# Kernel tuning notes

Hardware: AMD Instinct MI355X
Metric: run time of the kernel (lower is better)

## Reference

```python
import jax, jax.numpy as jnp
import numpy as np


def setup_inputs() -> dict:
    key = jax.random.key(0)
    kq, kk, kv = jax.random.split(key, 3)
    B, L, H, E = 4, 2048, 16, 64
    return {
        "queries": jax.random.normal(kq, (B, L, H, E), dtype=jnp.float32),
        "keys": jax.random.normal(kk, (B, L, H, E), dtype=jnp.float32),
        "values": jax.random.normal(kv, (B, L, H, E), dtype=jnp.float32),
    }


def reference(queries, keys, values):
    B, L, H, E = queries.shape
    S = keys.shape[1]
    scale = 1.0 / jnp.sqrt(jnp.asarray(E, queries.dtype))
    # scores: [B, H, L, S]
    scores = jnp.einsum("blhe,bshe->bhls", queries, keys)
    # causal mask: disallow s > l (upper triangle, diagonal=1)
    causal = jnp.triu(jnp.ones((L, S), dtype=bool), k=1)
    scores = jnp.where(causal[None, None], -jnp.inf, scores)
    A = jax.nn.softmax(scale * scores, axis=-1)
    V = jnp.einsum("bhls,bshd->blhd", A, values)
    return V
```

## Files before the change

### kernel.cpp

```cpp
#include <hip/hip_runtime.h>
#include <hip/hip_bf16.h>

typedef __attribute__((ext_vector_type(8))) short short8;
typedef __attribute__((ext_vector_type(4))) float f32x4;
typedef __attribute__((ext_vector_type(4))) float f4;
typedef __attribute__((ext_vector_type(2))) unsigned uint2v;
typedef __attribute__((ext_vector_type(4))) unsigned uint4v;

#define MFMA(a, b, c) __builtin_amdgcn_mfma_f32_16x16x32_bf16(a, b, c, 0, 0, 0)

constexpr int B_ = 4, L = 2048, H = 16, E = 64;
constexpr int QBLK = 128, KVBLK = 64, NW = 8;
constexpr int LDP = 72;
constexpr float LOG2E = 1.4426950408889634f;
constexpr float C2 = 14.426950408889634f;
constexpr size_t NELEM = (size_t)B_ * L * H * E;
constexpr size_t WS_NEEDED = NELEM * 2 * 2;
constexpr int TILE_SHORTS = KVBLK * E;

__device__ __forceinline__ unsigned short f2bf(float f) {
  union { float f; unsigned u; } x;
  x.f = f;
  unsigned r = x.u + 0x7fffu + ((x.u >> 16) & 1u);
  return (unsigned short)(r >> 16);
}

__device__ __forceinline__ float exp2_fast(float x) {
  float r;
  asm("v_exp_f32 %0, %1" : "=v"(r) : "v"(x));
  return r;
}
__device__ __forceinline__ unsigned cvt_pk_bf16(float lo, float hi) {
  unsigned r;
  asm("v_cvt_pk_bf16_f32 %0, %1, %2" : "=v"(r) : "v"(lo), "v"(hi));
  return r;
}

__device__ __forceinline__ void gload_lds16(const void* g, void* l) {
  __builtin_amdgcn_global_load_lds(
      (const __attribute__((address_space(1))) unsigned*)g,
      (__attribute__((address_space(3))) unsigned*)l, 16, 0, 0);
}

__device__ __forceinline__ void stage_tile8(const unsigned short* gtile,
                                            unsigned short* ltile,
                                            unsigned qb, unsigned qs) {
  gload_lds16((const char*)gtile + qs, (char*)ltile + qb);
}

__device__ __forceinline__ void barrier_raw() {
  __builtin_amdgcn_sched_barrier(0);
  __builtin_amdgcn_s_barrier();
  __builtin_amdgcn_sched_barrier(0);
}

__global__ __launch_bounds__(256)
void prep_all(const float* __restrict__ K, const float* __restrict__ V,
              unsigned short* __restrict__ Kb, unsigned short* __restrict__ Vt) {
  __shared__ unsigned short Ts[E][KVBLK + 8];
  const int tid = threadIdx.x;
  if (blockIdx.y == 0) {
    const size_t t = (size_t)blockIdx.x * 256 + tid;
    const size_t row = t >> 3;
    const int e0 = ((int)t & 7) * 8;
    const int h = (int)(row % H);
    const size_t bl = row / H;
    const int l = (int)(bl % L);
    const int b = (int)(bl / L);
    f4 a = *(const f4*)(K + t * 8);
    f4 c = *(const f4*)(K + t * 8 + 4);
    short8 o;
    o[0] = (short)f2bf(a[0]); o[1] = (short)f2bf(a[1]);
    o[2] = (short)f2bf(a[2]); o[3] = (short)f2bf(a[3]);
    o[4] = (short)f2bf(c[0]); o[5] = (short)f2bf(c[1]);
    o[6] = (short)f2bf(c[2]); o[7] = (short)f2bf(c[3]);
    *(short8*)(Kb + (((size_t)b * H + h) * L + l) * E + e0) = o;
    return;
  }
  const int blk = blockIdx.x;
  if (blk >= B_ * H * (L / KVBLK)) return;
  const int st = blk % (L / KVBLK);
  const int bh = blk / (L / KVBLK);
  const int h = bh % H, b = bh / H;
  const int r = tid >> 3, e0 = (tid & 7) * 8;
  const float* vp = V + (((size_t)b * L + st * KVBLK) * H + h) * E;
#pragma unroll
  for (int rr = 0; rr < 2; ++rr) {
    const int row = rr * 32 + r;
    f4 a = *(const f4*)(vp + (size_t)row * (H * E) + e0);
    f4 c = *(const f4*)(vp + (size_t)row * (H * E) + e0 + 4);
#pragma unroll
    for (int j = 0; j < 4; ++j) Ts[e0 + j][row] = f2bf(a[j]);
#pragma unroll
    for (int j = 0; j < 4; ++j) Ts[e0 + 4 + j][row] = f2bf(c[j]);
  }
  __syncthreads();
  const int e = tid >> 2, k0 = (tid & 3) * 16;
  unsigned short* op = Vt + ((size_t)bh * (L / KVBLK) + st) * (E * KVBLK) + e * KVBLK + k0;
  *(short8*)op = *(const short8*)&Ts[e][k0];
  *(short8*)(op + 8) = *(const short8*)&Ts[e][k0 + 8];
}

__global__ __launch_bounds__(512, 6)
void fattn3(const float* __restrict__ Q, const unsigned short* __restrict__ Kb,
            const unsigned short* __restrict__ Vt, float* __restrict__ O) {
  const int bh = blockIdx.x;
  const int y = blockIdx.y;
  const int r4 = y >> 2, x4 = y & 3;
  const int qtile = (3 - r4) * 4 + ((x4 + r4) & 3);
  const int b = bh >> 4, h = bh & 15;
  const int tid = threadIdx.x;
  const int wid = tid >> 6;
  const int lane = tid & 63;
  const int lg = lane >> 4, lm = lane & 15;
  const int qrow0 = qtile * QBLK + wid * 16;

  __shared__ __align__(16) unsigned short Ks[2][TILE_SHORTS];
  __shared__ __align__(16) unsigned short Vs[2][TILE_SHORTS];
  __shared__ __align__(16) unsigned short Pt[NW][16 * LDP];

  const unsigned sqb = (unsigned)wid * 1024u + (unsigned)lane * 16u;
  const unsigned sqs = sqb ^ (((sqb >> 7) & 7u) << 4);

  const unsigned short* kbase = Kb + (size_t)bh * L * E;
  const unsigned short* vbase = Vt + (size_t)bh * L * E;

  stage_tile8(kbase, Ks[0], sqb, sqs);
  stage_tile8(vbase, Vs[0], sqb, sqs);

  int offA[4], offB[4];
#pragma unroll
  for (int ct = 0; ct < 4; ++ct) {
    const int row = ct * 16 + lm;
    offA[ct] = row * 128 + ((lg ^ (row & 7)) << 4);
    offB[ct] = row * 128 + (((4 + lg) ^ (row & 7)) << 4);
  }
  int wrOff[4];
#pragma unroll
  for (int ct = 0; ct < 4; ++ct) wrOff[ct] = (lm * LDP + ct * 16 + lg * 4) * 2;
  const int rdOff0 = (lm * LDP + lg * 8) * 2;
  const int rdOff1 = (lm * LDP + 32 + lg * 8) * 2;
  char* const ptw = (char*)Pt[wid];

  short8 qf0, qf1;
  {
    const float qsc = 0.125f * LOG2E;
    const float* qp = Q + (((size_t)b * L + qrow0 + lm) * H + h) * E + lg * 8;
    f4 a0 = *(const f4*)(qp);
    f4 a1 = *(const f4*)(qp + 4);
    f4 b0 = *(const f4*)(qp + 32);
    f4 b1 = *(const f4*)(qp + 36);
    uint4v u0 = { cvt_pk_bf16(a0[0] * qsc, a0[1] * qsc),
                  cvt_pk_bf16(a0[2] * qsc, a0[3] * qsc),
                  cvt_pk_bf16(a1[0] * qsc, a1[1] * qsc),
                  cvt_pk_bf16(a1[2] * qsc, a1[3] * qsc) };
    uint4v u1 = { cvt_pk_bf16(b0[0] * qsc, b0[1] * qsc),
                  cvt_pk_bf16(b0[2] * qsc, b0[3] * qsc),
                  cvt_pk_bf16(b1[0] * qsc, b1[1] * qsc),
                  cvt_pk_bf16(b1[2] * qsc, b1[3] * qsc) };
    qf0 = __builtin_bit_cast(short8, u0);
    qf1 = __builtin_bit_cast(short8, u1);
  }

  f32x4 o[4];
#pragma unroll
  for (int et = 0; et < 4; ++et) o[et] = (f32x4){0.f, 0.f, 0.f, 0.f};
  float lsum = 0.f;

  const int nkv = 2 * qtile + 2;
  const f32x4 cinit = (f32x4){-C2, -C2, -C2, -C2};

  for (int kt = 0; kt < nkv; ++kt) {
    const int cur = kt & 1, nxt = cur ^ 1;

    asm volatile("s_waitcnt lgkmcnt(0)" ::: "memory");
    barrier_raw();

    if (kt + 1 < nkv) {
      stage_tile8(kbase + (size_t)(kt + 1) * TILE_SHORTS, Ks[nxt], sqb, sqs);
      stage_tile8(vbase + (size_t)(kt + 1) * TILE_SHORTS, Vs[nxt], sqb, sqs);
      asm volatile("s_waitcnt vmcnt(2)" ::: "memory");
    } else {
      asm volatile("s_waitcnt vmcnt(0)" ::: "memory");
    }
    barrier_raw();

    const bool dead = (kt * KVBLK) > (qrow0 + 15);
    if (dead) continue;

    const char* kl = (const char*)Ks[cur];
    const char* vl = (const char*)Vs[cur];

    f32x4 stl[4];
#pragma unroll
    for (int ct = 0; ct < 4; ++ct) {
      short8 k0f = *(const short8*)(kl + offA[ct]);
      short8 k1f = *(const short8*)(kl + offB[ct]);
      f32x4 acc = cinit;
      acc = MFMA(k0f, qf0, acc);
      acc = MFMA(k1f, qf1, acc);
      stl[ct] = acc;
    }

    if (kt * KVBLK + KVBLK - 1 > qrow0) {
#pragma unroll
      for (int ct = 0; ct < 4; ++ct)
#pragma unroll
        for (int r = 0; r < 4; ++r) {
          const int key = kt * KVBLK + ct * 16 + lg * 4 + r;
          if (key > qrow0 + lm) stl[ct][r] = -1e30f;
        }
    }

#pragma unroll
    for (int ct = 0; ct < 4; ++ct)
#pragma unroll
      for (int r = 0; r < 4; ++r) {
        const float p = exp2_fast(stl[ct][r]);
        stl[ct][r] = p;
        lsum += p;
      }

#pragma unroll
    for (int ct = 0; ct < 4; ++ct) {
      uint2v w;
      w[0] = cvt_pk_bf16(stl[ct][0], stl[ct][1]);
      w[1] = cvt_pk_bf16(stl[ct][2], stl[ct][3]);
      *(uint2v*)(ptw + wrOff[ct]) = w;
    }
    short8 pf0 = *(const short8*)(ptw + rdOff0);
    short8 pf1 = *(const short8*)(ptw + rdOff1);

#pragma unroll
    for (int et = 0; et < 4; ++et) {
      short8 v0 = *(const short8*)(vl + offA[et]);
      short8 v1 = *(const short8*)(vl + offB[et]);
      o[et] = MFMA(pf0, v0, o[et]);
      o[et] = MFMA(pf1, v1, o[et]);
    }
  }

  lsum += __shfl_xor(lsum, 16);
  lsum += __shfl_xor(lsum, 32);
  float linv[4];
#pragma unroll
  for (int r = 0; r < 4; ++r) linv[r] = 1.f / __shfl(lsum, lg * 20 + r);
  float* op = O + (((size_t)b * L + qrow0 + lg * 4) * H + h) * E;
#pragma unroll
  for (int r = 0; r < 4; ++r)
#pragma unroll
    for (int et = 0; et < 4; ++et)
      op[(size_t)r * (H * E) + et * 16 + lm] = o[et][r] * linv[r];
}

constexpr int LDV_F = 72, LDP_F = 72;
__global__ __launch_bounds__(256, 2)
void fattn_v1(const float* __restrict__ Q, const float* __restrict__ K,
              const float* __restrict__ V, float* __restrict__ O) {
  const int qtile = blockIdx.x;
  const int bh = blockIdx.y;
  const int b = bh / H, h = bh % H;
  const int tid = threadIdx.x;
  const int wid = tid >> 6;
  const int lane = tid & 63;
  const int lg = lane >> 4, lm = lane & 15;
  __shared__ __align__(16) short Vs[E * LDV_F];
  __shared__ __align__(16) short Ps[4][16 * LDP_F];
  const int qrow0 = qtile * 64 + wid * 16;
  short8 qf[2];
  {
    const float* qp = Q + (((size_t)b * L + (qrow0 + lm)) * H + h) * E + lg * 8;
#pragma unroll
    for (int kc = 0; kc < 2; ++kc) {
      f4 a = *(const f4*)(qp + kc * 32);
      f4 c = *(const f4*)(qp + kc * 32 + 4);
      short8 r;
      r[0] = (short)f2bf(a[0] * 0.125f); r[1] = (short)f2bf(a[1] * 0.125f);
      r[2] = (short)f2bf(a[2] * 0.125f); r[3] = (short)f2bf(a[3] * 0.125f);
      r[4] = (short)f2bf(c[0] * 0.125f); r[5] = (short)f2bf(c[1] * 0.125f);
      r[6] = (short)f2bf(c[2] * 0.125f); r[7] = (short)f2bf(c[3] * 0.125f);
      qf[kc] = r;
    }
  }
  f32x4 o[4];
#pragma unroll
  for (int et = 0; et < 4; ++et) o[et] = (f32x4){0.f, 0.f, 0.f, 0.f};
  float mrow[4], lrow[4];
#pragma unroll
  for (int r = 0; r < 4; ++r) { mrow[r] = -1e30f; lrow[r] = 0.f; }
  const float* kbase = K + (((size_t)b * L) * H + h) * E;
  const float* vbase = V + (((size_t)b * L) * H + h) * E;
  const int nkv = qtile + 1;
  for (int kt = 0; kt < nkv; ++kt) {
    __syncthreads();
    {
      const int key = tid >> 2;
      const int eb = (tid & 3) * 16;
      const float* vp = vbase + (size_t)(kt * 64 + key) * (H * E) + eb;
#pragma unroll
      for (int i = 0; i < 4; ++i) {
        f4 v = *(const f4*)(vp + i * 4);
        Vs[(eb + i * 4 + 0) * LDV_F + key] = (short)f2bf(v[0]);
        Vs[(eb + i * 4 + 1) * LDV_F + key] = (short)f2bf(v[1]);
        Vs[(eb + i * 4 + 2) * LDV_F + key] = (short)f2bf(v[2]);
        Vs[(eb + i * 4 + 3) * LDV_F + key] = (short)f2bf(v[3]);
      }
    }
    f32x4 s[4];
#pragma unroll
    for (int ct = 0; ct < 4; ++ct) {
      f32x4 acc = (f32x4){0.f, 0.f, 0.f, 0.f};
      const float* kp = kbase + (size_t)(kt * 64 + ct * 16 + lm) * (H * E) + lg * 8;
#pragma unroll
      for (int kc = 0; kc < 2; ++kc) {
        f4 a = *(const f4*)(kp + kc * 32);
        f4 c = *(const f4*)(kp + kc * 32 + 4);
        short8 kf;
        kf[0] = (short)f2bf(a[0]); kf[1] = (short)f2bf(a[1]);
        kf[2] = (short)f2bf(a[2]); kf[3] = (short)f2bf(a[3]);
        kf[4] = (short)f2bf(c[0]); kf[5] = (short)f2bf(c[1]);
        kf[6] = (short)f2bf(c[2]); kf[7] = (short)f2bf(c[3]);
        acc = MFMA(qf[kc], kf, acc);
      }
      s[ct] = acc;
    }
    if (kt == nkv - 1) {
#pragma unroll
      for (int ct = 0; ct < 4; ++ct) {
        const int sg = kt * 64 + ct * 16 + lm;
#pragma unroll
        for (int r = 0; r < 4; ++r)
          if (sg > qrow0 + lg * 4 + r) s[ct][r] = -1e30f;
      }
    }
#pragma unroll
    for (int r = 0; r < 4; ++r) {
      float tm = fmaxf(fmaxf(s[0][r], s[1][r]), fmaxf(s[2][r], s[3][r]));
      tm = fmaxf(tm, __shfl_xor(tm, 1));
      tm = fmaxf(tm, __shfl_xor(tm, 2));
      tm = fmaxf(tm, __shfl_xor(tm, 4));
      tm = fmaxf(tm, __shfl_xor(tm, 8));
      const float mnew = fmaxf(mrow[r], tm);
      const float sc = __expf(mrow[r] - mnew);
      mrow[r] = mnew;
      float rs = 0.f;
#pragma unroll
      for (int ct = 0; ct < 4; ++ct) {
        const float p = __expf(s[ct][r] - mnew);
        s[ct][r] = p;
        rs += p;
      }
      rs += __shfl_xor(rs, 1);
      rs += __shfl_xor(rs, 2);
      rs += __shfl_xor(rs, 4);
      rs += __shfl_xor(rs, 8);
      lrow[r] = lrow[r] * sc + rs;
#pragma unroll
      for (int et = 0; et < 4; ++et) o[et][r] *= sc;
    }
#pragma unroll
    for (int ct = 0; ct < 4; ++ct)
#pragma unroll
      for (int r = 0; r < 4; ++r)
        Ps[wid][(lg * 4 + r) * LDP_F + ct * 16 + lm] = (short)f2bf(s[ct][r]);
    __syncthreads();
    short8 pf[2];
    pf[0] = *(const short8*)&Ps[wid][lm * LDP_F + 0 * 32 + lg * 8];
    pf[1] = *(const short8*)&Ps[wid][lm * LDP_F + 1 * 32 + lg * 8];
#pragma unroll
    for (int et = 0; et < 4; ++et)
#pragma unroll
      for (int kc = 0; kc < 2; ++kc) {
        short8 vf = *(const short8*)&Vs[(et * 16 + lm) * LDV_F + kc * 32 + lg * 8];
        o[et] = MFMA(pf[kc], vf, o[et]);
      }
  }
  float* op = O + (((size_t)b * L + qrow0) * H + h) * E;
#pragma unroll
  for (int r = 0; r < 4; ++r) {
    const float inv = 1.f / lrow[r];
#pragma unroll
    for (int et = 0; et < 4; ++et)
      op[(size_t)(lg * 4 + r) * (H * E) + et * 16 + lm] = o[et][r] * inv;
  }
}

extern "C" void kernel_launch(void* const* d_in, const int* in_sizes, int n_in,
                              void* d_out, int out_size, void* d_ws, size_t ws_size,
                              hipStream_t stream) {
  const float* Q = (const float*)d_in[0];
  const float* K = (const float*)d_in[1];
  const float* V = (const float*)d_in[2];
  float* Out = (float*)d_out;
  if (ws_size >= WS_NEEDED) {
    unsigned short* Kb = (unsigned short*)d_ws;
    unsigned short* Vt = Kb + NELEM;
    dim3 gp((unsigned)(NELEM / (256 * 8)), 2);
    prep_all<<<gp, 256, 0, stream>>>(K, V, Kb, Vt);
    dim3 grid(B_ * H, L / QBLK);
    fattn3<<<grid, 512, 0, stream>>>(Q, Kb, Vt, Out);
  } else {
    dim3 grid(L / 64, B_ * H);
    fattn_v1<<<grid, 256, 0, stream>>>(Q, K, V, Out);
  }
}
```

Baseline: 70.34 us.

## Process two 128-row query slices per block to reuse staged K/V tiles

Raises the query tile per block from 128 to 256 rows, so each wave holds two 16-row query fragments and two accumulator sets. Every K/V tile staged in shared memory is then used by both slices. This halves the global K/V traffic and barrier overhead per query row. In exchange the grid halves to 512 blocks, per-thread register use rises (launch bounds lowered to 4), and the heaviest causal block now walks twice as many KV tiles, which lengthens the critical path.

```diff
diff --git a/kernel.cpp b/kernel.cpp
--- a/kernel.cpp
+++ b/kernel.cpp
@@ -10,7 +10,7 @@
 #define MFMA(a, b, c) __builtin_amdgcn_mfma_f32_16x16x32_bf16(a, b, c, 0, 0, 0)
 
 constexpr int B_ = 4, L = 2048, H = 16, E = 64;
-constexpr int QBLK = 128, KVBLK = 64, NW = 8;
+constexpr int QBLK2 = 256, KVBLK = 64, NW = 8;
 constexpr int LDP = 72;
 constexpr float LOG2E = 1.4426950408889634f;
 constexpr float C2 = 14.426950408889634f;
@@ -101,19 +101,20 @@
   *(short8*)(op + 8) = *(const short8*)&Ts[e][k0 + 8];
 }
 
-__global__ __launch_bounds__(512, 6)
-void fattn3(const float* __restrict__ Q, const unsigned short* __restrict__ Kb,
+__global__ __launch_bounds__(512, 4)
+void fattn4(const float* __restrict__ Q, const unsigned short* __restrict__ Kb,
             const unsigned short* __restrict__ Vt, float* __restrict__ O) {
   const int bh = blockIdx.x;
   const int y = blockIdx.y;
   const int r4 = y >> 2, x4 = y & 3;
-  const int qtile = (3 - r4) * 4 + ((x4 + r4) & 3);
+  const int qtile = r4 ? x4 : 7 - x4;
   const int b = bh >> 4, h = bh & 15;
   const int tid = threadIdx.x;
   const int wid = tid >> 6;
   const int lane = tid & 63;
   const int lg = lane >> 4, lm = lane & 15;
-  const int qrow0 = qtile * QBLK + wid * 16;
+  const int qrowA = qtile * QBLK2 + wid * 16;
+  const int qrowB = qrowA + 128;
 
   __shared__ __align__(16) unsigned short Ks[2][TILE_SHORTS];
   __shared__ __align__(16) unsigned short Vs[2][TILE_SHORTS];
@@ -142,32 +143,50 @@
   const int rdOff1 = (lm * LDP + 32 + lg * 8) * 2;
   char* const ptw = (char*)Pt[wid];
 
-  short8 qf0, qf1;
+  short8 qfA0, qfA1, qfB0, qfB1;
   {
     const float qsc = 0.125f * LOG2E;
-    const float* qp = Q + (((size_t)b * L + qrow0 + lm) * H + h) * E + lg * 8;
-    f4 a0 = *(const f4*)(qp);
-    f4 a1 = *(const f4*)(qp + 4);
-    f4 b0 = *(const f4*)(qp + 32);
-    f4 b1 = *(const f4*)(qp + 36);
-    uint4v u0 = { cvt_pk_bf16(a0[0] * qsc, a0[1] * qsc),
-                  cvt_pk_bf16(a0[2] * qsc, a0[3] * qsc),
-                  cvt_pk_bf16(a1[0] * qsc, a1[1] * qsc),
-                  cvt_pk_bf16(a1[2] * qsc, a1[3] * qsc) };
-    uint4v u1 = { cvt_pk_bf16(b0[0] * qsc, b0[1] * qsc),
-                  cvt_pk_bf16(b0[2] * qsc, b0[3] * qsc),
-                  cvt_pk_bf16(b1[0] * qsc, b1[1] * qsc),
-                  cvt_pk_bf16(b1[2] * qsc, b1[3] * qsc) };
-    qf0 = __builtin_bit_cast(short8, u0);
-    qf1 = __builtin_bit_cast(short8, u1);
-  }
-
-  f32x4 o[4];
-#pragma unroll
-  for (int et = 0; et < 4; ++et) o[et] = (f32x4){0.f, 0.f, 0.f, 0.f};
-  float lsum = 0.f;
-
-  const int nkv = 2 * qtile + 2;
+    const float* qpA = Q + (((size_t)b * L + qrowA + lm) * H + h) * E + lg * 8;
+    const float* qpB = Q + (((size_t)b * L + qrowB + lm) * H + h) * E + lg * 8;
+    f4 a0 = *(const f4*)(qpA);
+    f4 a1 = *(const f4*)(qpA + 4);
+    f4 a2 = *(const f4*)(qpA + 32);
+    f4 a3 = *(const f4*)(qpA + 36);
+    f4 b0 = *(const f4*)(qpB);
+    f4 b1 = *(const f4*)(qpB + 4);
+    f4 b2 = *(const f4*)(qpB + 32);
+    f4 b3 = *(const f4*)(qpB + 36);
+    uint4v uA0 = { cvt_pk_bf16(a0[0] * qsc, a0[1] * qsc),
+                   cvt_pk_bf16(a0[2] * qsc, a0[3] * qsc),
+                   cvt_pk_bf16(a1[0] * qsc, a1[1] * qsc),
+                   cvt_pk_bf16(a1[2] * qsc, a1[3] * qsc) };
+    uint4v uA1 = { cvt_pk_bf16(a2[0] * qsc, a2[1] * qsc),
+                   cvt_pk_bf16(a2[2] * qsc, a2[3] * qsc),
+                   cvt_pk_bf16(a3[0] * qsc, a3[1] * qsc),
+                   cvt_pk_bf16(a3[2] * qsc, a3[3] * qsc) };
+    uint4v uB0 = { cvt_pk_bf16(b0[0] * qsc, b0[1] * qsc),
+                   cvt_pk_bf16(b0[2] * qsc, b0[3] * qsc),
+                   cvt_pk_bf16(b1[0] * qsc, b1[1] * qsc),
+                   cvt_pk_bf16(b1[2] * qsc, b1[3] * qsc) };
+    uint4v uB1 = { cvt_pk_bf16(b2[0] * qsc, b2[1] * qsc),
+                   cvt_pk_bf16(b2[2] * qsc, b2[3] * qsc),
+                   cvt_pk_bf16(b3[0] * qsc, b3[1] * qsc),
+                   cvt_pk_bf16(b3[2] * qsc, b3[3] * qsc) };
+    qfA0 = __builtin_bit_cast(short8, uA0);
+    qfA1 = __builtin_bit_cast(short8, uA1);
+    qfB0 = __builtin_bit_cast(short8, uB0);
+    qfB1 = __builtin_bit_cast(short8, uB1);
+  }
+
+  f32x4 oA[4], oB[4];
+#pragma unroll
+  for (int et = 0; et < 4; ++et) {
+    oA[et] = (f32x4){0.f, 0.f, 0.f, 0.f};
+    oB[et] = (f32x4){0.f, 0.f, 0.f, 0.f};
+  }
+  float lsumA = 0.f, lsumB = 0.f;
+
+  const int nkv = 4 * qtile + 4;
   const f32x4 cinit = (f32x4){-C2, -C2, -C2, -C2};
 
   for (int kt = 0; kt < nkv; ++kt) {
@@ -185,72 +204,122 @@
     }
     barrier_raw();
 
-    const bool dead = (kt * KVBLK) > (qrow0 + 15);
-    if (dead) continue;
-
     const char* kl = (const char*)Ks[cur];
     const char* vl = (const char*)Vs[cur];
-
-    f32x4 stl[4];
-#pragma unroll
-    for (int ct = 0; ct < 4; ++ct) {
-      short8 k0f = *(const short8*)(kl + offA[ct]);
-      short8 k1f = *(const short8*)(kl + offB[ct]);
-      f32x4 acc = cinit;
-      acc = MFMA(k0f, qf0, acc);
-      acc = MFMA(k1f, qf1, acc);
-      stl[ct] = acc;
-    }
-
-    if (kt * KVBLK + KVBLK - 1 > qrow0) {
+    const int key0 = kt * KVBLK;
+
+    if (key0 <= qrowA + 15) {
+      f32x4 stl[4];
+#pragma unroll
+      for (int ct = 0; ct < 4; ++ct) {
+        short8 k0f = *(const short8*)(kl + offA[ct]);
+        short8 k1f = *(const short8*)(kl + offB[ct]);
+        f32x4 acc = cinit;
+        acc = MFMA(k0f, qfA0, acc);
+        acc = MFMA(k1f, qfA1, acc);
+        stl[ct] = acc;
+      }
+      if (key0 + KVBLK - 1 > qrowA) {
+#pragma unroll
+        for (int ct = 0; ct < 4; ++ct)
+#pragma unroll
+          for (int r = 0; r < 4; ++r) {
+            const int key = key0 + ct * 16 + lg * 4 + r;
+            if (key > qrowA + lm) stl[ct][r] = -1e30f;
+          }
+      }
 #pragma unroll
       for (int ct = 0; ct < 4; ++ct)
 #pragma unroll
         for (int r = 0; r < 4; ++r) {
-          const int key = kt * KVBLK + ct * 16 + lg * 4 + r;
-          if (key > qrow0 + lm) stl[ct][r] = -1e30f;
+          const float p = exp2_fast(stl[ct][r]);
+          stl[ct][r] = p;
+          lsumA += p;
         }
-    }
-
-#pragma unroll
-    for (int ct = 0; ct < 4; ++ct)
-#pragma unroll
-      for (int r = 0; r < 4; ++r) {
-        const float p = exp2_fast(stl[ct][r]);
-        stl[ct][r] = p;
-        lsum += p;
-      }
-
-#pragma unroll
-    for (int ct = 0; ct < 4; ++ct) {
-      uint2v w;
-      w[0] = cvt_pk_bf16(stl[ct][0], stl[ct][1]);
-      w[1] = cvt_pk_bf16(stl[ct][2], stl[ct][3]);
-      *(uint2v*)(ptw + wrOff[ct]) = w;
-    }
-    short8 pf0 = *(const short8*)(ptw + rdOff0);
-    short8 pf1 = *(const short8*)(ptw + rdOff1);
-
+#pragma unroll
+      for (int ct = 0; ct < 4; ++ct) {
+        uint2v w;
+        w[0] = cvt_pk_bf16(stl[ct][0], stl[ct][1]);
+        w[1] = cvt_pk_bf16(stl[ct][2], stl[ct][3]);
+        *(uint2v*)(ptw + wrOff[ct]) = w;
+      }
+      short8 pf0 = *(const short8*)(ptw + rdOff0);
+      short8 pf1 = *(const short8*)(ptw + rdOff1);
+#pragma unroll
+      for (int et = 0; et < 4; ++et) {
+        short8 v0 = *(const short8*)(vl + offA[et]);
+        short8 v1 = *(const short8*)(vl + offB[et]);
+        oA[et] = MFMA(pf0, v0, oA[et]);
+        oA[et] = MFMA(pf1, v1, oA[et]);
+      }
+    }
+
+    if (key0 <= qrowB + 15) {
+      f32x4 stl[4];
+#pragma unroll
+      for (int ct = 0; ct < 4; ++ct) {
+        short8 k0f = *(const short8*)(kl + offA[ct]);
+        short8 k1f = *(const short8*)(kl + offB[ct]);
+        f32x4 acc = cinit;
+        acc = MFMA(k0f, qfB0, acc);
+        acc = MFMA(k1f, qfB1, acc);
+        stl[ct] = acc;
+      }
+      if (key0 + KVBLK - 1 > qrowB) {
+#pragma unroll
+        for (int ct = 0; ct < 4; ++ct)
+#pragma unroll
+          for (int r = 0; r < 4; ++r) {
+            const int key = key0 + ct * 16 + lg * 4 + r;
+            if (key > qrowB + lm) stl[ct][r] = -1e30f;
+          }
+      }
+#pragma unroll
+      for (int ct = 0; ct < 4; ++ct)
+#pragma unroll
+        for (int r = 0; r < 4; ++r) {
+          const float p = exp2_fast(stl[ct][r]);
+          stl[ct][r] = p;
+          lsumB += p;
+        }
+#pragma unroll
+      for (int ct = 0; ct < 4; ++ct) {
+        uint2v w;
+        w[0] = cvt_pk_bf16(stl[ct][0], stl[ct][1]);
+        w[1] = cvt_pk_bf16(stl[ct][2], stl[ct][3]);
+        *(uint2v*)(ptw + wrOff[ct]) = w;
+      }
+      short8 pf0 = *(const short8*)(ptw + rdOff0);
+      short8 pf1 = *(const short8*)(ptw + rdOff1);
+#pragma unroll
+      for (int et = 0; et < 4; ++et) {
+        short8 v0 = *(const short8*)(vl + offA[et]);
+        short8 v1 = *(const short8*)(vl + offB[et]);
+        oB[et] = MFMA(pf0, v0, oB[et]);
+        oB[et] = MFMA(pf1, v1, oB[et]);
+      }
+    }
+  }
+
+  lsumA += __shfl_xor(lsumA, 16);
+  lsumA += __shfl_xor(lsumA, 32);
+  lsumB += __shfl_xor(lsumB, 16);
+  lsumB += __shfl_xor(lsumB, 32);
+  float linvA[4], linvB[4];
+#pragma unroll
+  for (int r = 0; r < 4; ++r) {
+    linvA[r] = 1.f / __shfl(lsumA, lg * 20 + r);
+    linvB[r] = 1.f / __shfl(lsumB, lg * 20 + r);
+  }
+  float* opA = O + (((size_t)b * L + qrowA + lg * 4) * H + h) * E;
+  float* opB = O + (((size_t)b * L + qrowB + lg * 4) * H + h) * E;
+#pragma unroll
+  for (int r = 0; r < 4; ++r)
 #pragma unroll
     for (int et = 0; et < 4; ++et) {
-      short8 v0 = *(const short8*)(vl + offA[et]);
-      short8 v1 = *(const short8*)(vl + offB[et]);
-      o[et] = MFMA(pf0, v0, o[et]);
-      o[et] = MFMA(pf1, v1, o[et]);
-    }
-  }
-
-  lsum += __shfl_xor(lsum, 16);
-  lsum += __shfl_xor(lsum, 32);
-  float linv[4];
-#pragma unroll
-  for (int r = 0; r < 4; ++r) linv[r] = 1.f / __shfl(lsum, lg * 20 + r);
-  float* op = O + (((size_t)b * L + qrow0 + lg * 4) * H + h) * E;
-#pragma unroll
-  for (int r = 0; r < 4; ++r)
-#pragma unroll
-    for (int et = 0; et < 4; ++et)
-      op[(size_t)r * (H * E) + et * 16 + lm] = o[et][r] * linv[r];
+      opA[(size_t)r * (H * E) + et * 16 + lm] = oA[et][r] * linvA[r];
+      opB[(size_t)r * (H * E) + et * 16 + lm] = oB[et][r] * linvB[r];
+    }
 }
 
 constexpr int LDV_F = 72, LDP_F = 72;
@@ -397,8 +466,8 @@
     unsigned short* Vt = Kb + NELEM;
     dim3 gp((unsigned)(NELEM / (256 * 8)), 2);
     prep_all<<<gp, 256, 0, stream>>>(K, V, Kb, Vt);
-    dim3 grid(B_ * H, L / QBLK);
-    fattn3<<<grid, 512, 0, stream>>>(Q, Kb, Vt, Out);
+    dim3 grid(B_ * H, L / QBLK2);
+    fattn4<<<grid, 512, 0, stream>>>(Q, Kb, Vt, Out);
   } else {
     dim3 grid(L / 64, B_ * H);
     fattn_v1<<<grid, 256, 0, stream>>>(Q, K, V, Out);
```

Result: slower. 76.92 us (+9.3%).
